# Performance work log

Hardware: AMD Instinct MI355X
Metric: run time of the kernel (lower is better)

## Reference

```python
import jax, jax.numpy as jnp
import numpy as np

T, H, I, E, K = 1024, 1024, 1024, 16, 8
INIT_STD = 0.02


def setup_inputs() -> dict:
    key = jax.random.key(0)
    k0, k1, k2, k3, k4 = jax.random.split(key, 5)
    hidden_states = jax.random.normal(k0, (T, H), dtype=jnp.float32)
    top_k_index = jax.random.randint(k1, (T, K), 0, E, dtype=jnp.int64)
    top_k_weights = jax.random.uniform(k2, (T, K), dtype=jnp.float32)
    gate_up_proj = jax.random.normal(k3, (E, 2 * I, H), dtype=jnp.float32) * INIT_STD
    down_proj = jax.random.normal(k4, (E, H, I), dtype=jnp.float32) * INIT_STD
    return {
        "hidden_states": hidden_states,
        "top_k_index": top_k_index,
        "top_k_weights": top_k_weights,
        "gate_up_proj": gate_up_proj,
        "down_proj": down_proj,
    }


def reference(hidden_states, top_k_index, top_k_weights, gate_up_proj, down_proj):
    # hidden_states: [T, H]; gate_up_proj: [E, 2I, H]; down_proj: [E, H, I]
    num_tokens = hidden_states.shape[0]
    num_experts = gate_up_proj.shape[0]

    # Per-token combine weights: scatter top_k_weights into a dense [T, E] map.
    # Tokens not routed to expert e get weight 0, so the dense all-expert
    # compute below is mathematically identical to the masked gather/scatter loop.
    token_ids = jnp.arange(num_tokens)[:, None]  # [T, 1]
    combine = jnp.zeros((num_tokens, num_experts), dtype=hidden_states.dtype)
    combine = combine.at[token_ids, top_k_index].add(top_k_weights)  # [T, E]

    # Gated MLP for every (token, expert) pair.
    gate_up = jnp.einsum("th,eoh->teo", hidden_states, gate_up_proj)  # [T, E, 2I]
    gate, up = jnp.split(gate_up, 2, axis=-1)
    act = jax.nn.silu(gate) * up  # [T, E, I]
    down = jnp.einsum("tei,ehi->teh", act, down_proj)  # [T, E, H]

    # Weighted combine over experts (zero weight -> no contribution).
    return jnp.einsum("teh,te->th", down, combine)  # [T, H]
```

## Files before the change

### kernel.cpp

```cpp
#include <hip/hip_runtime.h>
#include <cstdint>
#include <cstddef>

#define TT 1024
#define HH 1024
#define IW 1024
#define EE 16
#define KK 8
#define NSLOT (TT*KK)
#define NTMAX 80

typedef unsigned short u16;
typedef unsigned int   u32;
typedef __attribute__((ext_vector_type(4))) float f32x4;
typedef __attribute__((ext_vector_type(8))) short s16x8;
typedef __attribute__((ext_vector_type(8))) u16   u16x8;

__device__ __forceinline__ u16 f2bf(float f) {
  union { float f; u32 u; } v; v.f = f;
  u32 u = v.u + 0x7fffu + ((v.u >> 16) & 1u);
  return (u16)(u >> 16);
}
__device__ __forceinline__ float bf2f(u16 b) {
  union { u32 u; float f; } v; v.u = (u32)b << 16;
  return v.f;
}

__device__ __forceinline__ void gload16(const void* g, void* l) {
  __builtin_amdgcn_global_load_lds(
      (const __attribute__((address_space(1))) u32*)g,
      (__attribute__((address_space(3))) u32*)l, 16, 0, 0);
}

#define MFMA16(a, b, c) __builtin_amdgcn_mfma_f32_16x16x32_bf16((a), (b), (c), 0, 0, 0)


__global__ void k_cvt_all(const float* __restrict__ hs, const float* __restrict__ gup,
                          const float* __restrict__ dp, u16* __restrict__ xb,
                          u16* __restrict__ gupb, u16* __restrict__ dpb) {
  int b = blockIdx.x;
  const float* src; u16* dst; size_t rel;
  if (b < 512)        { src = hs;  dst = xb;   rel = (size_t)b; }
  else if (b < 16896) { src = gup; dst = gupb; rel = (size_t)(b - 512); }
  else                { src = dp;  dst = dpb;  rel = (size_t)(b - 16896); }
  size_t g = rel * 2048 + (size_t)threadIdx.x * 8;
  const f32x4* s = (const f32x4*)(src + g);
  f32x4 f0 = s[0], f1 = s[1];
  u16x8 p;
#pragma unroll
  for (int i = 0; i < 4; ++i) { p[i] = f2bf(f0[i]); p[i + 4] = f2bf(f1[i]); }
  *(u16x8*)(dst + g) = p;
}


__global__ void k_route(const int* __restrict__ idx, const float* __restrict__ tkw,
                        int* __restrict__ offsets, int* __restrict__ slot_token,
                        float* __restrict__ slot_w, int* __restrict__ inv,
                        int* __restrict__ tile_e, int* __restrict__ tile_mt) {
  __shared__ int cnt[EE], cur[EE];
  const int tid = threadIdx.x;
  if (tid < EE) cnt[tid] = 0;
  __syncthreads();
  for (int s = tid; s < NSLOT; s += 256) atomicAdd(&cnt[idx[s]], 1);
  __syncthreads();
  if (tid == 0) {
    int r = 0, t = 0;
    for (int e = 0; e < EE; ++e) {
      offsets[e] = r; cur[e] = r;
      int c = cnt[e];
      for (int mt = 0; mt * 128 < c; ++mt) { tile_e[t] = e; tile_mt[t] = mt; ++t; }
      r += c;
    }
    offsets[EE] = r;
    for (; t < NTMAX; ++t) tile_e[t] = -1;
  }
  __syncthreads();
  for (int s = tid; s < NSLOT; s += 256) {
    int e = idx[s];
    int pos = atomicAdd(&cur[e], 1);
    slot_token[pos] = s >> 3;
    slot_w[pos] = tkw[s];
    inv[s] = pos;
  }
}


#define G1_ASZ (128*32)
#define G1_BSZ (64*32)

__global__ __launch_bounds__(256, 2) void k_gemm1(
    const u16* __restrict__ xb,
    const u16* __restrict__ gupb,
    const int* __restrict__ offsets,
    const int* __restrict__ slot_token,
    const float* __restrict__ slot_w,
    const int* __restrict__ tile_e,
    const int* __restrict__ tile_mt,
    u16* __restrict__ act)
{
  __shared__ __align__(16) u16 As[2 * G1_ASZ];
  __shared__ __align__(16) u16 Bgs[2 * G1_BSZ];
  __shared__ __align__(16) u16 Bus[2 * G1_BSZ];

  const int e = tile_e[blockIdx.y];
  if (e < 0) return;
  const int mt = tile_mt[blockIdx.y], nt = blockIdx.x;
  const int off = offsets[e];
  const int ne  = offsets[e + 1] - off;

  const int tid = threadIdx.x;
  const int lane = tid & 63, wid = tid >> 6;
  const int wm = wid >> 1, wn = wid & 1;

  const int l4 = lane >> 2;
  const int lq = lane & 3;
  const int chunk = lq ^ ((l4 >> 1) & 3);

  const u16* asrc[2];
#pragma unroll
  for (int q = 0; q < 2; ++q) {
    int grow = mt * 128 + q * 64 + wid * 16 + l4;
    if (grow >= ne) grow = ne - 1;
    asrc[q] = xb + (size_t)slot_token[off + grow] * HH + chunk * 8;
  }
  const int bch = nt * 64 + wid * 16 + l4;
  const u16* bgsrc = gupb + ((size_t)e * 2 * IW + bch) * HH + chunk * 8;
  const u16* busrc = bgsrc + (size_t)IW * HH;
  const int ad0 = (0 * 64 + wid * 16) * 32;
  const int ad1 = (1 * 64 + wid * 16) * 32;
  const int bd  = (wid * 16) * 32;

  f32x4 accg[4][2], accu[4][2];
  const f32x4 zz = {0.f, 0.f, 0.f, 0.f};
#pragma unroll
  for (int m = 0; m < 4; ++m)
#pragma unroll
    for (int n = 0; n < 2; ++n) { accg[m][n] = zz; accu[m][n] = zz; }

  const int r16 = lane & 15, kg = lane >> 4;
  const int rq = ((kg ^ ((r16 >> 1) & 3)) << 3);

  gload16(asrc[0], As + ad0);
  gload16(asrc[1], As + ad1);
  gload16(bgsrc,   Bgs + bd);
  gload16(busrc,   Bus + bd);
  __syncthreads();

  for (int kk = 0; kk < HH / 32; ++kk) {
    const int cur = kk & 1;
    if (kk + 1 < HH / 32) {
      const int nb = cur ^ 1, k0 = (kk + 1) * 32;
      gload16(asrc[0] + k0, As + nb * G1_ASZ + ad0);
      gload16(asrc[1] + k0, As + nb * G1_ASZ + ad1);
      gload16(bgsrc   + k0, Bgs + nb * G1_BSZ + bd);
      gload16(busrc   + k0, Bus + nb * G1_BSZ + bd);
    }
    const u16* Ab  = As  + cur * G1_ASZ;
    const u16* Bgb = Bgs + cur * G1_BSZ;
    const u16* Bub = Bus + cur * G1_BSZ;

    s16x8 a[4], bg[2], bu[2];
#pragma unroll
    for (int m = 0; m < 4; ++m)
      a[m] = *(const s16x8*)(Ab + (wm * 64 + m * 16 + r16) * 32 + rq);
#pragma unroll
    for (int n = 0; n < 2; ++n) {
      bg[n] = *(const s16x8*)(Bgb + (wn * 32 + n * 16 + r16) * 32 + rq);
      bu[n] = *(const s16x8*)(Bub + (wn * 32 + n * 16 + r16) * 32 + rq);
    }
#pragma unroll
    for (int m = 0; m < 4; ++m)
#pragma unroll
      for (int n = 0; n < 2; ++n) {
        accg[m][n] = MFMA16(a[m], bg[n], accg[m][n]);
        accu[m][n] = MFMA16(a[m], bu[n], accu[m][n]);
      }
    __syncthreads();
  }

#pragma unroll
  for (int m = 0; m < 4; ++m) {
    const int baserow = mt * 128 + wm * 64 + m * 16 + kg * 4;
#pragma unroll
    for (int n = 0; n < 2; ++n) {
      const int c = nt * 64 + wn * 32 + n * 16 + r16;
#pragma unroll
      for (int j = 0; j < 4; ++j) {
        const int row = baserow + j;
        if (row < ne) {
          float g = accg[m][n][j], u = accu[m][n][j];
          float sv = g / (1.f + __expf(-g));
          act[(size_t)(off + row) * IW + c] = f2bf(sv * u * slot_w[off + row]);
        }
      }
    }
  }
}


#define G2_SZ (128*32)

__global__ __launch_bounds__(256, 2) void k_gemm2(
    const u16* __restrict__ act,
    const u16* __restrict__ dpb,
    const int* __restrict__ offsets,
    const int* __restrict__ tile_e,
    const int* __restrict__ tile_mt,
    u16* __restrict__ wdown)
{
  __shared__ __align__(16) u16 As[2 * G2_SZ];
  __shared__ __align__(16) u16 Bs[2 * G2_SZ];

  const int e = tile_e[blockIdx.y];
  if (e < 0) return;
  const int mt = tile_mt[blockIdx.y], nt = blockIdx.x;
  const int off = offsets[e];
  const int ne  = offsets[e + 1] - off;

  const int tid = threadIdx.x;
  const int lane = tid & 63, wid = tid >> 6;
  const int wm = wid >> 1, wn = wid & 1;

  const int l4 = lane >> 2, lq = lane & 3;
  const int chunk = lq ^ ((l4 >> 1) & 3);

  const u16* asrc[2];
#pragma unroll
  for (int q = 0; q < 2; ++q) {
    int grow = mt * 128 + q * 64 + wid * 16 + l4;
    if (grow >= ne) grow = ne - 1;
    asrc[q] = act + (size_t)(off + grow) * IW + chunk * 8;
  }
  const u16* bsrc[2];
#pragma unroll
  for (int q = 0; q < 2; ++q)
    bsrc[q] = dpb + ((size_t)e * HH + nt * 128 + q * 64 + wid * 16 + l4) * IW + chunk * 8;

  const int d0 = (0 * 64 + wid * 16) * 32;
  const int d1 = (1 * 64 + wid * 16) * 32;

  f32x4 acc[4][4];
  const f32x4 zz = {0.f, 0.f, 0.f, 0.f};
#pragma unroll
  for (int m = 0; m < 4; ++m)
#pragma unroll
    for (int n = 0; n < 4; ++n) acc[m][n] = zz;

  const int r16 = lane & 15, kg = lane >> 4;
  const int rq = ((kg ^ ((r16 >> 1) & 3)) << 3);

  gload16(asrc[0], As + d0);
  gload16(asrc[1], As + d1);
  gload16(bsrc[0], Bs + d0);
  gload16(bsrc[1], Bs + d1);
  __syncthreads();

  for (int kk = 0; kk < IW / 32; ++kk) {
    const int cur = kk & 1;
    if (kk + 1 < IW / 32) {
      const int nb = cur ^ 1, k0 = (kk + 1) * 32;
      gload16(asrc[0] + k0, As + nb * G2_SZ + d0);
      gload16(asrc[1] + k0, As + nb * G2_SZ + d1);
      gload16(bsrc[0] + k0, Bs + nb * G2_SZ + d0);
      gload16(bsrc[1] + k0, Bs + nb * G2_SZ + d1);
    }
    const u16* Ab = As + cur * G2_SZ;
    const u16* Bb = Bs + cur * G2_SZ;

    s16x8 a[4], b[4];
#pragma unroll
    for (int m = 0; m < 4; ++m)
      a[m] = *(const s16x8*)(Ab + (wm * 64 + m * 16 + r16) * 32 + rq);
#pragma unroll
    for (int n = 0; n < 4; ++n)
      b[n] = *(const s16x8*)(Bb + (wn * 64 + n * 16 + r16) * 32 + rq);
#pragma unroll
    for (int m = 0; m < 4; ++m)
#pragma unroll
      for (int n = 0; n < 4; ++n)
        acc[m][n] = MFMA16(a[m], b[n], acc[m][n]);
    __syncthreads();
  }

#pragma unroll
  for (int m = 0; m < 4; ++m) {
    const int baserow = mt * 128 + wm * 64 + m * 16 + kg * 4;
#pragma unroll
    for (int n = 0; n < 4; ++n) {
      const int h = nt * 128 + wn * 64 + n * 16 + r16;
#pragma unroll
      for (int j = 0; j < 4; ++j) {
        const int row = baserow + j;
        if (row < ne)
          wdown[(size_t)(off + row) * HH + h] = f2bf(acc[m][n][j]);
      }
    }
  }
}


__global__ void k_combine(const u16* __restrict__ wdown, const int* __restrict__ inv,
                          float* __restrict__ out) {
  int g = blockIdx.x * 256 + threadIdx.x;
  int t = g >> 7;
  int hv = (g & 127) * 8;
  const int* ip = inv + t * KK;
  float acc[8] = {0.f, 0.f, 0.f, 0.f, 0.f, 0.f, 0.f, 0.f};
#pragma unroll
  for (int k = 0; k < KK; ++k) {
    int pos = ip[k];
    u16x8 v = *(const u16x8*)(wdown + (size_t)pos * HH + hv);
#pragma unroll
    for (int j = 0; j < 8; ++j) acc[j] += bf2f(v[j]);
  }
  f32x4 o0 = {acc[0], acc[1], acc[2], acc[3]};
  f32x4 o1 = {acc[4], acc[5], acc[6], acc[7]};
  *(f32x4*)(out + (size_t)t * HH + hv)     = o0;
  *(f32x4*)(out + (size_t)t * HH + hv + 4) = o1;
}


extern "C" void kernel_launch(void* const* d_in, const int* in_sizes, int n_in,
                              void* d_out, int out_size, void* d_ws, size_t ws_size,
                              hipStream_t stream) {
  const float* hs  = (const float*)d_in[0];
  const int*   idx = (const int*)d_in[1];
  const float* tkw = (const float*)d_in[2];
  const float* gup = (const float*)d_in[3];
  const float* dpw = (const float*)d_in[4];
  float* out = (float*)d_out;

  char* ws = (char*)d_ws;
  size_t o = 0;
  u16* xb   = (u16*)(ws + o);       o += (size_t)TT * HH * 2;
  u16* gupb = (u16*)(ws + o);       o += (size_t)EE * 2 * IW * HH * 2;
  u16* dpb  = (u16*)(ws + o);       o += (size_t)EE * HH * IW * 2;
  int* offsets = (int*)(ws + o);    o += 128;
  int* tile_e  = (int*)(ws + o);    o += NTMAX * 4;
  int* tile_mt = (int*)(ws + o);    o += NTMAX * 4;
  int* slot_token = (int*)(ws + o); o += (size_t)NSLOT * 4;
  int* inv     = (int*)(ws + o);    o += (size_t)NSLOT * 4;
  float* slot_w = (float*)(ws + o); o += (size_t)NSLOT * 4;
  o = (o + 255) & ~(size_t)255;
  u16* act = (u16*)(ws + o);        o += (size_t)NSLOT * IW * 2;
  u16* wdown = (u16*)(ws + o);      o += (size_t)NSLOT * HH * 2;

  k_route<<<1, 256, 0, stream>>>(idx, tkw, offsets, slot_token, slot_w, inv,
                                 tile_e, tile_mt);
  k_cvt_all<<<25088, 256, 0, stream>>>(hs, gup, dpw, xb, gupb, dpb);
  k_gemm1<<<dim3(IW / 64, NTMAX), 256, 0, stream>>>(xb, gupb, offsets, slot_token,
                                                    slot_w, tile_e, tile_mt, act);
  k_gemm2<<<dim3(HH / 128, NTMAX), 256, 0, stream>>>(act, dpb, offsets, tile_e,
                                                     tile_mt, wdown);
  k_combine<<<TT * HH / 8 / 256, 256, 0, stream>>>(wdown, inv, out);
}
```

Baseline: 387.3 us.

## Triple-buffer GEMM k-loops with vmcnt waits and grid-stride the conversion kernel

Both grouped GEMM kernels move from double to triple LDS buffering. They prefetch two k-steps ahead and use one s_waitcnt vmcnt plus s_barrier per iteration in place of the trailing __syncthreads, so global loads overlap more MFMA work. Launch bounds rise to 3 blocks per CU to fit the larger LDS footprint. The fp32-to-bf16 conversion kernel is rewritten as a fixed 2048-block grid-stride loop in which each thread converts several 8-element chunks, cutting launch and scheduling overhead. The single barrier per iteration relies on the 3-buffer rotation to avoid write-after-read hazards, and the higher occupancy target may squeeze registers.

```diff
diff --git a/kernel.cpp b/kernel.cpp
--- a/kernel.cpp
+++ b/kernel.cpp
@@ -34,22 +34,31 @@
 
 #define MFMA16(a, b, c) __builtin_amdgcn_mfma_f32_16x16x32_bf16((a), (b), (c), 0, 0, 0)
 
+#define WAITBAR(N) asm volatile("s_waitcnt vmcnt(" #N ")\n\ts_barrier" ::: "memory")
+
+
+#define CVT_BLOCKS 2048
+#define CVT_STRIDE (CVT_BLOCKS * 256)
+
+__device__ __forceinline__ void cvt8(const float* __restrict__ s, u16* __restrict__ d,
+                                     size_t i) {
+  const f32x4* p = (const f32x4*)(s + i * 8);
+  f32x4 f0 = p[0], f1 = p[1];
+  u16x8 o;
+#pragma unroll
+  for (int j = 0; j < 4; ++j) { o[j] = f2bf(f0[j]); o[j + 4] = f2bf(f1[j]); }
+  *(u16x8*)(d + i * 8) = o;
+}
 
 __global__ void k_cvt_all(const float* __restrict__ hs, const float* __restrict__ gup,
                           const float* __restrict__ dp, u16* __restrict__ xb,
                           u16* __restrict__ gupb, u16* __restrict__ dpb) {
-  int b = blockIdx.x;
-  const float* src; u16* dst; size_t rel;
-  if (b < 512)        { src = hs;  dst = xb;   rel = (size_t)b; }
-  else if (b < 16896) { src = gup; dst = gupb; rel = (size_t)(b - 512); }
-  else                { src = dp;  dst = dpb;  rel = (size_t)(b - 16896); }
-  size_t g = rel * 2048 + (size_t)threadIdx.x * 8;
-  const f32x4* s = (const f32x4*)(src + g);
-  f32x4 f0 = s[0], f1 = s[1];
-  u16x8 p;
-#pragma unroll
-  for (int i = 0; i < 4; ++i) { p[i] = f2bf(f0[i]); p[i + 4] = f2bf(f1[i]); }
-  *(u16x8*)(dst + g) = p;
+  const int g = blockIdx.x * 256 + threadIdx.x;
+#pragma unroll
+  for (int i = 0; i < 8; ++i) cvt8(gup, gupb, (size_t)g + (size_t)i * CVT_STRIDE);
+#pragma unroll
+  for (int i = 0; i < 4; ++i) cvt8(dp, dpb, (size_t)g + (size_t)i * CVT_STRIDE);
+  if (g < 131072) cvt8(hs, xb, (size_t)g);
 }
 
 
@@ -87,8 +96,9 @@
 
 #define G1_ASZ (128*32)
 #define G1_BSZ (64*32)
-
-__global__ __launch_bounds__(256, 2) void k_gemm1(
+#define NK1 (HH/32)
+
+__global__ __launch_bounds__(256, 3) void k_gemm1(
     const u16* __restrict__ xb,
     const u16* __restrict__ gupb,
     const int* __restrict__ offsets,
@@ -98,9 +108,9 @@
     const int* __restrict__ tile_mt,
     u16* __restrict__ act)
 {
-  __shared__ __align__(16) u16 As[2 * G1_ASZ];
-  __shared__ __align__(16) u16 Bgs[2 * G1_BSZ];
-  __shared__ __align__(16) u16 Bus[2 * G1_BSZ];
+  __shared__ __align__(16) u16 As[3 * G1_ASZ];
+  __shared__ __align__(16) u16 Bgs[3 * G1_BSZ];
+  __shared__ __align__(16) u16 Bus[3 * G1_BSZ];
 
   const int e = tile_e[blockIdx.y];
   if (e < 0) return;
@@ -130,6 +140,14 @@
   const int ad1 = (1 * 64 + wid * 16) * 32;
   const int bd  = (wid * 16) * 32;
 
+#define STAGE1(k0, buf)                                   \
+  do {                                                    \
+    gload16(asrc[0] + (k0), As  + (buf) * G1_ASZ + ad0);  \
+    gload16(asrc[1] + (k0), As  + (buf) * G1_ASZ + ad1);  \
+    gload16(bgsrc   + (k0), Bgs + (buf) * G1_BSZ + bd);   \
+    gload16(busrc   + (k0), Bus + (buf) * G1_BSZ + bd);   \
+  } while (0)
+
   f32x4 accg[4][2], accu[4][2];
   const f32x4 zz = {0.f, 0.f, 0.f, 0.f};
 #pragma unroll
@@ -140,24 +158,15 @@
   const int r16 = lane & 15, kg = lane >> 4;
   const int rq = ((kg ^ ((r16 >> 1) & 3)) << 3);
 
-  gload16(asrc[0], As + ad0);
-  gload16(asrc[1], As + ad1);
-  gload16(bgsrc,   Bgs + bd);
-  gload16(busrc,   Bus + bd);
-  __syncthreads();
-
-  for (int kk = 0; kk < HH / 32; ++kk) {
-    const int cur = kk & 1;
-    if (kk + 1 < HH / 32) {
-      const int nb = cur ^ 1, k0 = (kk + 1) * 32;
-      gload16(asrc[0] + k0, As + nb * G1_ASZ + ad0);
-      gload16(asrc[1] + k0, As + nb * G1_ASZ + ad1);
-      gload16(bgsrc   + k0, Bgs + nb * G1_BSZ + bd);
-      gload16(busrc   + k0, Bus + nb * G1_BSZ + bd);
-    }
-    const u16* Ab  = As  + cur * G1_ASZ;
-    const u16* Bgb = Bgs + cur * G1_BSZ;
-    const u16* Bub = Bus + cur * G1_BSZ;
+  STAGE1(0, 0);
+  STAGE1(32, 1);
+  int cb = 0, pb = 2;
+  for (int kk = 0; kk < NK1; ++kk) {
+    if (kk + 1 < NK1) WAITBAR(4); else WAITBAR(0);
+    if (kk + 2 < NK1) STAGE1((kk + 2) * 32, pb);
+    const u16* Ab  = As  + cb * G1_ASZ;
+    const u16* Bgb = Bgs + cb * G1_BSZ;
+    const u16* Bub = Bus + cb * G1_BSZ;
 
     s16x8 a[4], bg[2], bu[2];
 #pragma unroll
@@ -175,8 +184,10 @@
         accg[m][n] = MFMA16(a[m], bg[n], accg[m][n]);
         accu[m][n] = MFMA16(a[m], bu[n], accu[m][n]);
       }
-    __syncthreads();
-  }
+    cb = (cb == 2) ? 0 : cb + 1;
+    pb = (pb == 2) ? 0 : pb + 1;
+  }
+#undef STAGE1
 
 #pragma unroll
   for (int m = 0; m < 4; ++m) {
@@ -199,8 +210,9 @@
 
 
 #define G2_SZ (128*32)
-
-__global__ __launch_bounds__(256, 2) void k_gemm2(
+#define NK2 (IW/32)
+
+__global__ __launch_bounds__(256, 3) void k_gemm2(
     const u16* __restrict__ act,
     const u16* __restrict__ dpb,
     const int* __restrict__ offsets,
@@ -208,8 +220,8 @@
     const int* __restrict__ tile_mt,
     u16* __restrict__ wdown)
 {
-  __shared__ __align__(16) u16 As[2 * G2_SZ];
-  __shared__ __align__(16) u16 Bs[2 * G2_SZ];
+  __shared__ __align__(16) u16 As[3 * G2_SZ];
+  __shared__ __align__(16) u16 Bs[3 * G2_SZ];
 
   const int e = tile_e[blockIdx.y];
   if (e < 0) return;
@@ -239,6 +251,14 @@
   const int d0 = (0 * 64 + wid * 16) * 32;
   const int d1 = (1 * 64 + wid * 16) * 32;
 
+#define STAGE2(k0, buf)                                  \
+  do {                                                   \
+    gload16(asrc[0] + (k0), As + (buf) * G2_SZ + d0);    \
+    gload16(asrc[1] + (k0), As + (buf) * G2_SZ + d1);    \
+    gload16(bsrc[0] + (k0), Bs + (buf) * G2_SZ + d0);    \
+    gload16(bsrc[1] + (k0), Bs + (buf) * G2_SZ + d1);    \
+  } while (0)
+
   f32x4 acc[4][4];
   const f32x4 zz = {0.f, 0.f, 0.f, 0.f};
 #pragma unroll
@@ -249,23 +269,14 @@
   const int r16 = lane & 15, kg = lane >> 4;
   const int rq = ((kg ^ ((r16 >> 1) & 3)) << 3);
 
-  gload16(asrc[0], As + d0);
-  gload16(asrc[1], As + d1);
-  gload16(bsrc[0], Bs + d0);
-  gload16(bsrc[1], Bs + d1);
-  __syncthreads();
-
-  for (int kk = 0; kk < IW / 32; ++kk) {
-    const int cur = kk & 1;
-    if (kk + 1 < IW / 32) {
-      const int nb = cur ^ 1, k0 = (kk + 1) * 32;
-      gload16(asrc[0] + k0, As + nb * G2_SZ + d0);
-      gload16(asrc[1] + k0, As + nb * G2_SZ + d1);
-      gload16(bsrc[0] + k0, Bs + nb * G2_SZ + d0);
-      gload16(bsrc[1] + k0, Bs + nb * G2_SZ + d1);
-    }
-    const u16* Ab = As + cur * G2_SZ;
-    const u16* Bb = Bs + cur * G2_SZ;
+  STAGE2(0, 0);
+  STAGE2(32, 1);
+  int cb = 0, pb = 2;
+  for (int kk = 0; kk < NK2; ++kk) {
+    if (kk + 1 < NK2) WAITBAR(4); else WAITBAR(0);
+    if (kk + 2 < NK2) STAGE2((kk + 2) * 32, pb);
+    const u16* Ab = As + cb * G2_SZ;
+    const u16* Bb = Bs + cb * G2_SZ;
 
     s16x8 a[4], b[4];
 #pragma unroll
@@ -279,8 +290,10 @@
 #pragma unroll
       for (int n = 0; n < 4; ++n)
         acc[m][n] = MFMA16(a[m], b[n], acc[m][n]);
-    __syncthreads();
-  }
+    cb = (cb == 2) ? 0 : cb + 1;
+    pb = (pb == 2) ? 0 : pb + 1;
+  }
+#undef STAGE2
 
 #pragma unroll
   for (int m = 0; m < 4; ++m) {
@@ -347,7 +360,7 @@
 
   k_route<<<1, 256, 0, stream>>>(idx, tkw, offsets, slot_token, slot_w, inv,
                                  tile_e, tile_mt);
-  k_cvt_all<<<25088, 256, 0, stream>>>(hs, gup, dpw, xb, gupb, dpb);
+  k_cvt_all<<<CVT_BLOCKS, 256, 0, stream>>>(hs, gup, dpw, xb, gupb, dpb);
   k_gemm1<<<dim3(IW / 64, NTMAX), 256, 0, stream>>>(xb, gupb, offsets, slot_token,
                                                     slot_w, tile_e, tile_mt, act);
   k_gemm2<<<dim3(HH / 128, NTMAX), 256, 0, stream>>>(act, dpb, offsets, tile_e,
```

After: 398.7 us. 3.0% more time.
